# Kernel optimization log

Hardware: AMD Instinct MI355X
Metric: run time of the kernel (lower is better)

The kernel has to match this reference:

```python
import jax, jax.numpy as jnp
import numpy as np

DIM = 256
NUM_HEADS = 4
WINDOW = 64
EPS = 1e-6


def setup_inputs() -> dict:
    key = jax.random.key(0)
    ks = jax.random.split(key, 12)
    d = DIM
    s = 0.02
    return {
        "x": jax.random.normal(ks[0], (4, 2049, d), dtype=jnp.float32),
        "norm1_w": jnp.ones((d,), jnp.float32),
        "in_proj_w": jax.random.normal(ks[1], (3 * d, d), jnp.float32) * s,
        "in_proj_b": jnp.zeros((3 * d,), jnp.float32),
        "out_proj_w": jax.random.normal(ks[2], (d, d), jnp.float32) * s,
        "out_proj_b": jnp.zeros((d,), jnp.float32),
        "norm2_w": jnp.ones((d,), jnp.float32),
        "w1": jax.random.normal(ks[3], (2 * d, d), jnp.float32) * s,
        "b1": jnp.zeros((2 * d,), jnp.float32),
        "w2": jax.random.normal(ks[4], (d, 2 * d), jnp.float32) * s,
        "b2": jnp.zeros((d,), jnp.float32),
    }


def _rmsnorm(x, w):
    r = jax.lax.rsqrt(jnp.mean(x * x, axis=-1, keepdims=True) + EPS)
    return x * r * w


def _factorized_mask(size):
    # global token 0 attends/attended everywhere; others banded within WINDOW
    idx = jnp.arange(size)
    band = jnp.abs(idx[:, None] - idx[None, :]) <= WINDOW
    allowed = band | (idx[:, None] == 0) | (idx[None, :] == 0)
    return jnp.where(allowed, 0.0, -jnp.inf).astype(jnp.float32)


def reference(x, norm1_w, in_proj_w, in_proj_b, out_proj_w, out_proj_b,
              norm2_w, w1, b1, w2, b2):
    B, S, D = x.shape
    H = NUM_HEADS
    dh = D // H
    residual = x
    h = _rmsnorm(x, norm1_w)
    # fused qkv projection (torch MHA in_proj): [B,S,3D]
    qkv = h @ in_proj_w.T + in_proj_b
    q, k, v = jnp.split(qkv, 3, axis=-1)
    q = q.reshape(B, S, H, dh).transpose(0, 2, 1, 3)  # [B,H,S,dh]
    k = k.reshape(B, S, H, dh).transpose(0, 2, 1, 3)
    v = v.reshape(B, S, H, dh).transpose(0, 2, 1, 3)
    scores = jnp.einsum("bhqd,bhkd->bhqk", q, k) / jnp.sqrt(jnp.float32(dh))
    scores = scores + _factorized_mask(S)  # additive -inf mask
    attn = jax.nn.softmax(scores, axis=-1)
    ctx = jnp.einsum("bhqk,bhkd->bhqd", attn, v)
    ctx = ctx.transpose(0, 2, 1, 3).reshape(B, S, D)
    attn_out = ctx @ out_proj_w.T + out_proj_b
    x1 = residual + attn_out
    h2 = _rmsnorm(x1, norm2_w)
    ffn = jax.nn.gelu(h2 @ w1.T + b1, approximate=False) @ w2.T + b2
    return x1 + ffn
```

## Files before the change

kernel.cpp:

```cpp
#include <hip/hip_runtime.h>
#include <hip/hip_bf16.h>
#include <math.h>

#define BATCH 4
#define SEQ 2049
#define DIMD 256
#define NHEAD 4
#define DH 64
#define WIN 64
#define M_ROWS (BATCH * SEQ)
#define M_PAD 8320

#define QBLK 33
#define NKB 10
#define PSTR 168
#define VGUARD 64
#define VW 2256

#define NSPLIT 33
#define TBLK 576

typedef __attribute__((ext_vector_type(8))) short short8;
typedef __attribute__((ext_vector_type(4))) float f32x4;
typedef __hip_bfloat16 bf16;

__device__ __forceinline__ float b2f(short u) {
    union { unsigned int i; float f; } c;
    c.i = ((unsigned int)(unsigned short)u) << 16;
    return c.f;
}
__device__ __forceinline__ short f2b(float f) {
    bf16 h = __float2bfloat16(f);
    return *reinterpret_cast<short*>(&h);
}

__global__ __launch_bounds__(256) void prep_kernel(
        const float* __restrict__ wq, const float* __restrict__ wo,
        const float* __restrict__ w1, const float* __restrict__ w2,
        bf16* __restrict__ oq, bf16* __restrict__ oo,
        bf16* __restrict__ o1, bf16* __restrict__ o2,
        const float* __restrict__ x, const float* __restrict__ nw,
        bf16* __restrict__ h) {
    const int bi = blockIdx.x, tid = threadIdx.x;
    if (bi < 2048) {
        int i = bi * 256 + tid;
        if (i < 196608)      oq[i]          = __float2bfloat16(wq[i]);
        else if (i < 262144) oo[i - 196608] = __float2bfloat16(wo[i - 196608]);
        else if (i < 393216) o1[i - 262144] = __float2bfloat16(w1[i - 262144]);
        else                 o2[i - 393216] = __float2bfloat16(w2[i - 393216]);
        return;
    }
    int wid = tid >> 6, lane = tid & 63;
    int row = (bi - 2048) * 4 + wid;
    if (row >= M_ROWS) return;
    const float4 v = reinterpret_cast<const float4*>(x + (size_t)row * DIMD)[lane];
    float ss = v.x * v.x + v.y * v.y + v.z * v.z + v.w * v.w;
    #pragma unroll
    for (int o = 1; o < 64; o <<= 1) ss += __shfl_xor(ss, o, 64);
    float r = rsqrtf(ss * (1.0f / DIMD) + 1e-6f);
    const float4 wv = reinterpret_cast<const float4*>(nw)[lane];
    bf16* hp = h + (size_t)row * DIMD + lane * 4;
    hp[0] = __float2bfloat16(v.x * r * wv.x);
    hp[1] = __float2bfloat16(v.y * r * wv.y);
    hp[2] = __float2bfloat16(v.z * r * wv.z);
    hp[3] = __float2bfloat16(v.w * r * wv.w);
}

__global__ __launch_bounds__(256) void rmsnorm_kernel(const float* __restrict__ x,
        const float* __restrict__ w, bf16* __restrict__ h, int M) {
    int wid = threadIdx.x >> 6, lane = threadIdx.x & 63;
    int row = blockIdx.x * 4 + wid;
    if (row >= M) return;
    const float4 v = reinterpret_cast<const float4*>(x + (size_t)row * DIMD)[lane];
    float ss = v.x * v.x + v.y * v.y + v.z * v.z + v.w * v.w;
    #pragma unroll
    for (int o = 1; o < 64; o <<= 1) ss += __shfl_xor(ss, o, 64);
    float r = rsqrtf(ss * (1.0f / DIMD) + 1e-6f);
    const float4 wv = reinterpret_cast<const float4*>(w)[lane];
    bf16* hp = h + (size_t)row * DIMD + lane * 4;
    hp[0] = __float2bfloat16(v.x * r * wv.x);
    hp[1] = __float2bfloat16(v.y * r * wv.y);
    hp[2] = __float2bfloat16(v.z * r * wv.z);
    hp[3] = __float2bfloat16(v.w * r * wv.w);
}

template<int MODE, int BN>
__global__ __launch_bounds__(256) void gemm_lds(
        const bf16* __restrict__ A, const bf16* __restrict__ B,
        const float* __restrict__ bias, const float* __restrict__ resid,
        void* __restrict__ C, int M, int N, int K) {
    constexpr int FN = BN / 32;
    __shared__ __align__(16) short lA[8 * 128 * 8];
    __shared__ __align__(16) short lB[8 * BN * 8];
    const int tid = threadIdx.x, lane = tid & 63, wid = tid >> 6;
    const int m0 = blockIdx.x * 128;
    const int n0 = blockIdx.y * BN;
    const int wr = wid >> 1, wc = wid & 1;
    const int r = lane & 15, g = lane >> 4;

    f32x4 acc[4][FN];
    #pragma unroll
    for (int i = 0; i < 4; i++)
        #pragma unroll
        for (int j = 0; j < FN; j++) acc[i][j] = (f32x4){0.f, 0.f, 0.f, 0.f};

    for (int k0 = 0; k0 < K; k0 += 64) {
        #pragma unroll
        for (int it = 0; it < 4; ++it) {
            int c = it * 256 + tid;
            int kc = c >> 7, row = c & 127;
            __builtin_amdgcn_global_load_lds(
                (const __attribute__((address_space(1))) void*)(A + (size_t)(m0 + row) * K + k0 + kc * 8),
                (__attribute__((address_space(3))) void*)&lA[c * 8], 16, 0, 0);
        }
        #pragma unroll
        for (int it = 0; it < BN / 32; ++it) {
            int c = it * 256 + tid;
            int kc = c / BN, row = c % BN;
            __builtin_amdgcn_global_load_lds(
                (const __attribute__((address_space(1))) void*)(B + (size_t)(n0 + row) * K + k0 + kc * 8),
                (__attribute__((address_space(3))) void*)&lB[c * 8], 16, 0, 0);
        }
        __syncthreads();

        #pragma unroll
        for (int kk = 0; kk < 2; kk++) {
            short8 a[4], b[FN];
            #pragma unroll
            for (int mi = 0; mi < 4; mi++)
                a[mi] = *reinterpret_cast<const short8*>(&lA[((kk * 4 + g) * 128 + wr * 64 + mi * 16 + r) * 8]);
            #pragma unroll
            for (int ni = 0; ni < FN; ni++)
                b[ni] = *reinterpret_cast<const short8*>(&lB[((kk * 4 + g) * BN + wc * (BN / 2) + ni * 16 + r) * 8]);
            #pragma unroll
            for (int mi = 0; mi < 4; mi++)
                #pragma unroll
                for (int ni = 0; ni < FN; ni++)
                    acc[mi][ni] = __builtin_amdgcn_mfma_f32_16x16x32_bf16(a[mi], b[ni], acc[mi][ni], 0, 0, 0);
        }
        __syncthreads();
    }

    const int c0 = lane & 15, r0 = (lane >> 4) * 4;
    #pragma unroll
    for (int mi = 0; mi < 4; mi++) {
        #pragma unroll
        for (int ni = 0; ni < FN; ni++) {
            int col = n0 + wc * (BN / 2) + ni * 16 + c0;
            float bv = bias[col];
            #pragma unroll
            for (int j = 0; j < 4; j++) {
                int row = m0 + wr * 64 + mi * 16 + r0 + j;
                if (row < M) {
                    float v = acc[mi][ni][j] + bv;
                    if (MODE == 2) v = 0.5f * v * (1.0f + erff(v * 0.70710678118654752f));
                    if (MODE == 1) {
                        v += resid[(size_t)row * N + col];
                        reinterpret_cast<float*>(C)[(size_t)row * N + col] = v;
                    } else {
                        reinterpret_cast<bf16*>(C)[(size_t)row * N + col] = __float2bfloat16(v);
                    }
                }
            }
        }
    }
}

__global__ __launch_bounds__(256) void trans_partial(const short* __restrict__ qkv,
                                                     short* __restrict__ vT,
                                                     float* __restrict__ part) {
    const int tid = threadIdx.x;
    if (blockIdx.x < TBLK) {
        __shared__ short tl[64][72];
        const int jt = blockIdx.x % 36, bh = blockIdx.x / 36;
        const int b = bh >> 2, h = bh & 3;
        const size_t rbase = (size_t)b * SEQ;
        const int cbase = jt * 64;
        #pragma unroll
        for (int it = 0; it < 2; it++) {
            int idx = it * 256 + tid;
            int jj = idx >> 3, dg = (idx & 7) * 8;
            int j = cbase + jj - VGUARD;
            short8 v = (short8){0, 0, 0, 0, 0, 0, 0, 0};
            if (j >= 0 && j < SEQ)
                v = *reinterpret_cast<const short8*>(qkv + (rbase + j) * 768 + 512 + h * 64 + dg);
            *reinterpret_cast<short8*>(&tl[jj][dg]) = v;
        }
        __syncthreads();
        #pragma unroll
        for (int it = 0; it < 2; it++) {
            int idx = it * 256 + tid;
            int d = idx >> 3, jg = (idx & 7) * 8;
            int c = cbase + jg;
            if (c + 8 <= VW) {
                short8 o;
                #pragma unroll
                for (int e = 0; e < 8; e++) o[e] = tl[jg + e][d];
                *reinterpret_cast<short8*>(vT + ((size_t)bh * 64 + d) * VW + c) = o;
            }
        }
        return;
    }
    __shared__ float q_s[64];
    __shared__ float p_s[64];
    __shared__ float meta[2];
    __shared__ float osum[4][64];
    const int idx = blockIdx.x - TBLK;
    const int bh = idx / NSPLIT, s = idx % NSPLIT;
    const int b = bh >> 2, h = bh & 3;
    const size_t base = (size_t)b * SEQ;
    const int j0 = s * 64;
    const int lane = tid & 63, wid = tid >> 6;

    if (tid < 64) q_s[tid] = b2f(qkv[base * 768 + h * 64 + tid]);
    __syncthreads();

    if (wid == 0) {
        int j = j0 + lane;
        float sc = -1e30f;
        if (j < SEQ) {
            const short8* kp = reinterpret_cast<const short8*>(qkv + (base + j) * 768 + 256 + h * 64);
            float acc = 0.f;
            #pragma unroll
            for (int d8 = 0; d8 < 8; ++d8) {
                short8 kv = kp[d8];
                #pragma unroll
                for (int e = 0; e < 8; ++e) acc += q_s[d8 * 8 + e] * b2f(kv[e]);
            }
            sc = acc * 0.125f;
        }
        float mx = sc;
        #pragma unroll
        for (int o = 1; o < 64; o <<= 1) mx = fmaxf(mx, __shfl_xor(mx, o, 64));
        float p = (j < SEQ) ? expf(sc - mx) : 0.f;
        p_s[lane] = p;
        float l = p;
        #pragma unroll
        for (int o = 1; o < 64; o <<= 1) l += __shfl_xor(l, o, 64);
        if (lane == 0) { meta[0] = mx; meta[1] = l; }
    }
    __syncthreads();

    float oa = 0.f;
    #pragma unroll
    for (int i0 = 0; i0 < 16; i0++) {
        int i = wid + i0 * 4;
        if (j0 + i < SEQ) oa += p_s[i] * b2f(qkv[(base + j0 + i) * 768 + 512 + h * 64 + lane]);
    }
    osum[wid][lane] = oa;
    __syncthreads();
    if (wid == 0) {
        float o = osum[0][lane] + osum[1][lane] + osum[2][lane] + osum[3][lane];
        float* pp = part + (size_t)(bh * NSPLIT + s) * 66;
        pp[lane] = o;
        if (lane == 0) { pp[64] = meta[0]; pp[65] = meta[1]; }
    }
}

__global__ __launch_bounds__(256) void attn_band_mfma(const short* __restrict__ qkv,
                                                      const short* __restrict__ vT,
                                                      const float* __restrict__ part,
                                                      short* __restrict__ ctx) {
    __shared__ short p_lds[4][16][PSTR];
    const int tid = threadIdx.x, lane = tid & 63, wid = tid >> 6;
    const int qb = blockIdx.x % QBLK;
    const int bh = blockIdx.x / QBLK;
    const int b = bh >> 2, h = bh & 3;
    const size_t rbase = (size_t)b * SEQ;
    const int q0w = qb * 64 + wid * 16;
    const int jbase = q0w - 64;
    const int lrow = lane & 15;
    const int koff = (lane >> 4) * 8;
    const int c0 = lrow, r0 = (lane >> 4) * 4;

    int qrow = q0w + lrow; if (qrow > SEQ - 1) qrow = SEQ - 1;
    const short* qp = qkv + (rbase + qrow) * 768 + h * 64;
    short8 aq0 = *reinterpret_cast<const short8*>(qp + koff);
    short8 aq1 = *reinterpret_cast<const short8*>(qp + 32 + koff);

    const short* k0p = qkv + rbase * 768 + 256 + h * 64;
    short8 k0a = *reinterpret_cast<const short8*>(k0p + koff);
    short8 k0b = *reinterpret_cast<const short8*>(k0p + 32 + koff);
    float s0 = 0.f;
    #pragma unroll
    for (int e = 0; e < 8; e++)
        s0 += b2f(aq0[e]) * b2f(k0a[e]) + b2f(aq1[e]) * b2f(k0b[e]);
    s0 += __shfl_xor(s0, 16, 64);
    s0 += __shfl_xor(s0, 32, 64);

    f32x4 s[NKB];
    #pragma unroll
    for (int n = 0; n < NKB; n++) {
        int j = jbase + n * 16 + lrow;
        int jc = j < 0 ? 0 : (j > SEQ - 1 ? SEQ - 1 : j);
        const short* kp = qkv + (rbase + jc) * 768 + 256 + h * 64;
        short8 bk0 = *reinterpret_cast<const short8*>(kp + koff);
        short8 bk1 = *reinterpret_cast<const short8*>(kp + 32 + koff);
        f32x4 acc = (f32x4){0.f, 0.f, 0.f, 0.f};
        acc = __builtin_amdgcn_mfma_f32_16x16x32_bf16(aq0, bk0, acc, 0, 0, 0);
        acc = __builtin_amdgcn_mfma_f32_16x16x32_bf16(aq1, bk1, acc, 0, 0, 0);
        s[n] = acc;
    }

    const float SC = 0.125f * 1.44269504088896340736f;
    const bool g1 = (jbase > 0);
    float s0q[4], m4[4];
    #pragma unroll
    for (int jj = 0; jj < 4; jj++) {
        s0q[jj] = __shfl(s0, r0 + jj, 64) * SC;
        m4[jj] = g1 ? s0q[jj] : -1e30f;
    }
    #pragma unroll
    for (int n = 0; n < NKB; n++) {
        int j = jbase + n * 16 + c0;
        bool jv = (j >= 0) && (j < SEQ);
        #pragma unroll
        for (int jj = 0; jj < 4; jj++) {
            int q = q0w + r0 + jj;
            int dd = q - j; if (dd < 0) dd = -dd;
            bool allowed = jv && (dd <= WIN || j == 0);
            float v = allowed ? s[n][jj] * SC : -1e30f;
            s[n][jj] = v;
            m4[jj] = fmaxf(m4[jj], v);
        }
    }
    #pragma unroll
    for (int o = 1; o < 16; o <<= 1) {
        #pragma unroll
        for (int jj = 0; jj < 4; jj++) m4[jj] = fmaxf(m4[jj], __shfl_xor(m4[jj], o, 64));
    }

    float p0[4], l4[4];
    #pragma unroll
    for (int jj = 0; jj < 4; jj++) {
        p0[jj] = g1 ? exp2f(s0q[jj] - m4[jj]) : 0.f;
        l4[jj] = p0[jj];
    }
    #pragma unroll
    for (int n = 0; n < NKB; n++) {
        #pragma unroll
        for (int jj = 0; jj < 4; jj++) {
            float p = exp2f(s[n][jj] - m4[jj]);
            l4[jj] += p;
            p_lds[wid][r0 + jj][n * 16 + c0] = f2b(p);
        }
    }
    #pragma unroll
    for (int o = 1; o < 16; o <<= 1) {
        #pragma unroll
        for (int jj = 0; jj < 4; jj++) l4[jj] += __shfl_xor(l4[jj], o, 64);
    }

    __syncthreads();

    f32x4 o[4];
    #pragma unroll
    for (int dn = 0; dn < 4; dn++) o[dn] = (f32x4){0.f, 0.f, 0.f, 0.f};
    #pragma unroll
    for (int ks = 0; ks < NKB / 2; ks++) {
        short8 ap = *reinterpret_cast<const short8*>(&p_lds[wid][lrow][ks * 32 + koff]);
        int cc = VGUARD + jbase + ks * 32 + koff;
        #pragma unroll
        for (int dn = 0; dn < 4; dn++) {
            short8 bv = *reinterpret_cast<const short8*>(
                vT + ((size_t)bh * 64 + dn * 16 + lrow) * VW + cc);
            o[dn] = __builtin_amdgcn_mfma_f32_16x16x32_bf16(ap, bv, o[dn], 0, 0, 0);
        }
    }

    #pragma unroll
    for (int jj = 0; jj < 4; jj++) {
        int q = q0w + r0 + jj;
        if (q >= 1 && q < SEQ) {
            float rl = 1.0f / l4[jj];
            #pragma unroll
            for (int dn = 0; dn < 4; dn++) {
                float v0 = b2f(qkv[rbase * 768 + 512 + h * 64 + dn * 16 + c0]);
                float val = (o[dn][jj] + p0[jj] * v0) * rl;
                ctx[(rbase + q) * 256 + h * 64 + dn * 16 + c0] = f2b(val);
            }
        }
    }

    if (qb == 0) {
        __syncthreads();
        if (wid == 0) {
            float m = (lane < NSPLIT) ? part[(size_t)(bh * NSPLIT + lane) * 66 + 64] : -1e30f;
            #pragma unroll
            for (int o2 = 1; o2 < 64; o2 <<= 1) m = fmaxf(m, __shfl_xor(m, o2, 64));
            float L = 0.f, ov = 0.f;
            for (int sp = 0; sp < NSPLIT; sp++) {
                const float* pp = part + (size_t)(bh * NSPLIT + sp) * 66;
                float w = expf(pp[64] - m);
                L += pp[65] * w;
                ov += pp[lane] * w;
            }
            ctx[rbase * 256 + h * 64 + lane] = f2b(ov / L);
        }
    }
}

extern "C" void kernel_launch(void* const* d_in, const int* in_sizes, int n_in,
                              void* d_out, int out_size, void* d_ws, size_t ws_size,
                              hipStream_t stream) {
    const float* x         = (const float*)d_in[0];
    const float* norm1_w   = (const float*)d_in[1];
    const float* in_proj_w = (const float*)d_in[2];
    const float* in_proj_b = (const float*)d_in[3];
    const float* out_proj_w= (const float*)d_in[4];
    const float* out_proj_b= (const float*)d_in[5];
    const float* norm2_w   = (const float*)d_in[6];
    const float* w1        = (const float*)d_in[7];
    const float* b1        = (const float*)d_in[8];
    const float* w2        = (const float*)d_in[9];
    const float* b2        = (const float*)d_in[10];
    float* out = (float*)d_out;

    const int M = M_ROWS;
    char* ws = (char*)d_ws;
    size_t off = 0;
    auto take = [&](size_t bytes) {
        char* p = ws + off;
        off = (off + bytes + 255) & ~(size_t)255;
        return p;
    };
    bf16* h_bf   = (bf16*)take((size_t)M_PAD * 256 * 2);
    bf16* qkv_bf = (bf16*)take((size_t)M_PAD * 768 * 2);
    bf16* ctx_bf = (bf16*)take((size_t)M_PAD * 256 * 2);
    float* x1    = (float*)take((size_t)M_PAD * 256 * 4);
    bf16* h2_bf  = (bf16*)take((size_t)M_PAD * 256 * 2);
    bf16* g_bf   = (bf16*)take((size_t)M_PAD * 512 * 2);
    bf16* wq_bf  = (bf16*)take(768 * 256 * 2);
    bf16* wo_bf  = (bf16*)take(256 * 256 * 2);
    bf16* w1_bf  = (bf16*)take(512 * 256 * 2);
    bf16* w2_bf  = (bf16*)take(256 * 512 * 2);
    float* part  = (float*)take((size_t)16 * NSPLIT * 66 * 4);
    short* vT    = (short*)take((size_t)16 * 64 * VW * 2);
    (void)ws_size; (void)in_sizes; (void)n_in; (void)out_size;

    prep_kernel<<<dim3(2048 + 2049), dim3(256), 0, stream>>>(
        in_proj_w, out_proj_w, w1, w2, wq_bf, wo_bf, w1_bf, w2_bf, x, norm1_w, h_bf);
    gemm_lds<0, 128><<<dim3(65, 6), dim3(256), 0, stream>>>(h_bf, wq_bf, in_proj_b, (const float*)nullptr,
                                                            (void*)qkv_bf, M, 768, 256);
    trans_partial<<<dim3(TBLK + 16 * NSPLIT), dim3(256), 0, stream>>>(
        (const short*)qkv_bf, vT, part);
    attn_band_mfma<<<dim3(16 * QBLK), dim3(256), 0, stream>>>(
        (const short*)qkv_bf, vT, part, (short*)ctx_bf);
    gemm_lds<1, 64><<<dim3(65, 4), dim3(256), 0, stream>>>(ctx_bf, wo_bf, out_proj_b, x,
                                                           (void*)x1, M, 256, 256);
    rmsnorm_kernel<<<dim3((M + 3) / 4), dim3(256), 0, stream>>>(x1, norm2_w, h2_bf, M);
    gemm_lds<2, 128><<<dim3(65, 4), dim3(256), 0, stream>>>(h2_bf, w1_bf, b1, (const float*)nullptr,
                                                            (void*)g_bf, M, 512, 256);
    gemm_lds<1, 64><<<dim3(65, 4), dim3(256), 0, stream>>>(g_bf, w2_bf, b2, x1,
                                                           (void*)out, M, 256, 512);
}
```

Measured before the change: 124.9 us.

## Fuse V transpose into QKV GEMM epilogue and RMSNorm into out-proj GEMM

The QKV GEMM epilogue now writes V straight into the transposed, guard-padded vT layout and writes Q/K to a narrower 512-wide buffer. This removes the separate transpose pass, and prep_kernel zeroes vT beforehand so the guard regions stay valid. The out-projection GEMM now uses full-row 32x256 tiles, so it can compute the residual add and the second RMSNorm in its epilogue, which drops the standalone rmsnorm kernel. In exchange, the V stores are scattered and uncoalesced, the out-proj grid has fewer blocks with a larger B tile per block, and prep does extra zeroing work.

New measurement: 127.8 us. +2.3%, slower.

```diff
diff --git a/kernel.cpp b/kernel.cpp
--- a/kernel.cpp
+++ b/kernel.cpp
@@ -5,8 +5,6 @@
 #define BATCH 4
 #define SEQ 2049
 #define DIMD 256
-#define NHEAD 4
-#define DH 64
 #define WIN 64
 #define M_ROWS (BATCH * SEQ)
 #define M_PAD 8320
@@ -16,9 +14,10 @@
 #define PSTR 168
 #define VGUARD 64
 #define VW 2256
+#define QKSTR 512
 
 #define NSPLIT 33
-#define TBLK 576
+#define VT_F4 288768
 
 typedef __attribute__((ext_vector_type(8))) short short8;
 typedef __attribute__((ext_vector_type(4))) float f32x4;
@@ -40,7 +39,7 @@
         bf16* __restrict__ oq, bf16* __restrict__ oo,
         bf16* __restrict__ o1, bf16* __restrict__ o2,
         const float* __restrict__ x, const float* __restrict__ nw,
-        bf16* __restrict__ h) {
+        bf16* __restrict__ h, float4* __restrict__ vTz) {
     const int bi = blockIdx.x, tid = threadIdx.x;
     if (bi < 2048) {
         int i = bi * 256 + tid;
@@ -50,6 +49,15 @@
         else                 o2[i - 393216] = __float2bfloat16(w2[i - 393216]);
         return;
     }
+    if (bi >= 4097) {
+        int zi = (bi - 4097) * 256 + tid;
+        #pragma unroll
+        for (int it = 0; it < 3; it++) {
+            int idx = zi + it * 512 * 256;
+            if (idx < VT_F4) vTz[idx] = (float4){0.f, 0.f, 0.f, 0.f};
+        }
+        return;
+    }
     int wid = tid >> 6, lane = tid & 63;
     int row = (bi - 2048) * 4 + wid;
     if (row >= M_ROWS) return;
@@ -66,22 +74,86 @@
     hp[3] = __float2bfloat16(v.w * r * wv.w);
 }
 
-__global__ __launch_bounds__(256) void rmsnorm_kernel(const float* __restrict__ x,
-        const float* __restrict__ w, bf16* __restrict__ h, int M) {
-    int wid = threadIdx.x >> 6, lane = threadIdx.x & 63;
-    int row = blockIdx.x * 4 + wid;
-    if (row >= M) return;
-    const float4 v = reinterpret_cast<const float4*>(x + (size_t)row * DIMD)[lane];
-    float ss = v.x * v.x + v.y * v.y + v.z * v.z + v.w * v.w;
-    #pragma unroll
-    for (int o = 1; o < 64; o <<= 1) ss += __shfl_xor(ss, o, 64);
-    float r = rsqrtf(ss * (1.0f / DIMD) + 1e-6f);
-    const float4 wv = reinterpret_cast<const float4*>(w)[lane];
-    bf16* hp = h + (size_t)row * DIMD + lane * 4;
-    hp[0] = __float2bfloat16(v.x * r * wv.x);
-    hp[1] = __float2bfloat16(v.y * r * wv.y);
-    hp[2] = __float2bfloat16(v.z * r * wv.z);
-    hp[3] = __float2bfloat16(v.w * r * wv.w);
+__global__ __launch_bounds__(256) void gemm_qkv(
+        const bf16* __restrict__ A, const bf16* __restrict__ B,
+        const float* __restrict__ bias, bf16* __restrict__ qk, short* __restrict__ vT) {
+    __shared__ __align__(16) short lA[8 * 128 * 8];
+    __shared__ __align__(16) short lB[8 * 128 * 8];
+    const int tid = threadIdx.x, lane = tid & 63, wid = tid >> 6;
+    const int m0 = blockIdx.x * 128;
+    const int n0 = blockIdx.y * 128;
+    const int wr = wid >> 1, wc = wid & 1;
+    const int r = lane & 15, g = lane >> 4;
+    const int K = 256;
+
+    f32x4 acc[4][4];
+    #pragma unroll
+    for (int i = 0; i < 4; i++)
+        #pragma unroll
+        for (int j = 0; j < 4; j++) acc[i][j] = (f32x4){0.f, 0.f, 0.f, 0.f};
+
+    for (int k0 = 0; k0 < K; k0 += 64) {
+        #pragma unroll
+        for (int it = 0; it < 4; ++it) {
+            int c = it * 256 + tid;
+            int kc = c >> 7, row = c & 127;
+            __builtin_amdgcn_global_load_lds(
+                (const __attribute__((address_space(1))) void*)(A + (size_t)(m0 + row) * K + k0 + kc * 8),
+                (__attribute__((address_space(3))) void*)&lA[c * 8], 16, 0, 0);
+        }
+        #pragma unroll
+        for (int it = 0; it < 4; ++it) {
+            int c = it * 256 + tid;
+            int kc = c >> 7, row = c & 127;
+            __builtin_amdgcn_global_load_lds(
+                (const __attribute__((address_space(1))) void*)(B + (size_t)(n0 + row) * K + k0 + kc * 8),
+                (__attribute__((address_space(3))) void*)&lB[c * 8], 16, 0, 0);
+        }
+        __syncthreads();
+        #pragma unroll
+        for (int kk = 0; kk < 2; kk++) {
+            short8 a[4], b[4];
+            #pragma unroll
+            for (int mi = 0; mi < 4; mi++)
+                a[mi] = *reinterpret_cast<const short8*>(&lA[((kk * 4 + g) * 128 + wr * 64 + mi * 16 + r) * 8]);
+            #pragma unroll
+            for (int ni = 0; ni < 4; ni++)
+                b[ni] = *reinterpret_cast<const short8*>(&lB[((kk * 4 + g) * 128 + wc * 64 + ni * 16 + r) * 8]);
+            #pragma unroll
+            for (int mi = 0; mi < 4; mi++)
+                #pragma unroll
+                for (int ni = 0; ni < 4; ni++)
+                    acc[mi][ni] = __builtin_amdgcn_mfma_f32_16x16x32_bf16(a[mi], b[ni], acc[mi][ni], 0, 0, 0);
+        }
+        __syncthreads();
+    }
+
+    const int c0 = lane & 15, r0 = (lane >> 4) * 4;
+    const bool isV = (n0 >= 512);
+    #pragma unroll
+    for (int mi = 0; mi < 4; mi++) {
+        #pragma unroll
+        for (int ni = 0; ni < 4; ni++) {
+            int col = n0 + wc * 64 + ni * 16 + c0;
+            float bv = bias[col];
+            #pragma unroll
+            for (int j = 0; j < 4; j++) {
+                int row = m0 + wr * 64 + mi * 16 + r0 + j;
+                if (row < M_ROWS) {
+                    float v = acc[mi][ni][j] + bv;
+                    if (!isV) {
+                        qk[(size_t)row * QKSTR + col] = __float2bfloat16(v);
+                    } else {
+                        int dcol = col - 512, hh = dcol >> 6, d = dcol & 63;
+                        int bb = row >> 11;
+                        int js = row - bb * SEQ;
+                        if (js < 0) { bb--; js += SEQ; }
+                        vT[((size_t)((bb * 4 + hh) * 64 + d)) * VW + VGUARD + js] = f2b(v);
+                    }
+                }
+            }
+        }
+    }
 }
 
 template<int MODE, int BN>
@@ -122,7 +194,6 @@
                 (__attribute__((address_space(3))) void*)&lB[c * 8], 16, 0, 0);
         }
         __syncthreads();
-
         #pragma unroll
         for (int kk = 0; kk < 2; kk++) {
             short8 a[4], b[FN];
@@ -166,60 +237,138 @@
     }
 }
 
-__global__ __launch_bounds__(256) void trans_partial(const short* __restrict__ qkv,
-                                                     short* __restrict__ vT,
-                                                     float* __restrict__ part) {
-    const int tid = threadIdx.x;
-    if (blockIdx.x < TBLK) {
-        __shared__ short tl[64][72];
-        const int jt = blockIdx.x % 36, bh = blockIdx.x / 36;
-        const int b = bh >> 2, h = bh & 3;
-        const size_t rbase = (size_t)b * SEQ;
-        const int cbase = jt * 64;
-        #pragma unroll
-        for (int it = 0; it < 2; it++) {
-            int idx = it * 256 + tid;
-            int jj = idx >> 3, dg = (idx & 7) * 8;
-            int j = cbase + jj - VGUARD;
-            short8 v = (short8){0, 0, 0, 0, 0, 0, 0, 0};
-            if (j >= 0 && j < SEQ)
-                v = *reinterpret_cast<const short8*>(qkv + (rbase + j) * 768 + 512 + h * 64 + dg);
-            *reinterpret_cast<short8*>(&tl[jj][dg]) = v;
+__global__ __launch_bounds__(256) void gemm_or(
+        const bf16* __restrict__ A, const bf16* __restrict__ B,
+        const float* __restrict__ bias, const float* __restrict__ resid,
+        const float* __restrict__ nw,
+        float* __restrict__ x1, bf16* __restrict__ h2) {
+    __shared__ __align__(16) short lA[8 * 32 * 8];
+    __shared__ __align__(16) short lB[8 * 256 * 8];
+    __shared__ float osq[4][32];
+    const int tid = threadIdx.x, lane = tid & 63, wid = tid >> 6;
+    const int m0 = blockIdx.x * 32;
+    const int wc = wid;
+    const int r = lane & 15, g = lane >> 4;
+    const int K = 256;
+
+    f32x4 acc[2][4];
+    #pragma unroll
+    for (int i = 0; i < 2; i++)
+        #pragma unroll
+        for (int j = 0; j < 4; j++) acc[i][j] = (f32x4){0.f, 0.f, 0.f, 0.f};
+
+    for (int k0 = 0; k0 < K; k0 += 64) {
+        {
+            int c = tid;
+            int kc = c >> 5, row = c & 31;
+            __builtin_amdgcn_global_load_lds(
+                (const __attribute__((address_space(1))) void*)(A + (size_t)(m0 + row) * K + k0 + kc * 8),
+                (__attribute__((address_space(3))) void*)&lA[c * 8], 16, 0, 0);
+        }
+        #pragma unroll
+        for (int it = 0; it < 8; ++it) {
+            int c = it * 256 + tid;
+            int kc = c >> 8, row = c & 255;
+            __builtin_amdgcn_global_load_lds(
+                (const __attribute__((address_space(1))) void*)(B + (size_t)row * K + k0 + kc * 8),
+                (__attribute__((address_space(3))) void*)&lB[c * 8], 16, 0, 0);
         }
         __syncthreads();
         #pragma unroll
-        for (int it = 0; it < 2; it++) {
-            int idx = it * 256 + tid;
-            int d = idx >> 3, jg = (idx & 7) * 8;
-            int c = cbase + jg;
-            if (c + 8 <= VW) {
-                short8 o;
+        for (int kk = 0; kk < 2; kk++) {
+            short8 a[2], b[4];
+            #pragma unroll
+            for (int mi = 0; mi < 2; mi++)
+                a[mi] = *reinterpret_cast<const short8*>(&lA[((kk * 4 + g) * 32 + mi * 16 + r) * 8]);
+            #pragma unroll
+            for (int ni = 0; ni < 4; ni++)
+                b[ni] = *reinterpret_cast<const short8*>(&lB[((kk * 4 + g) * 256 + wc * 64 + ni * 16 + r) * 8]);
+            #pragma unroll
+            for (int mi = 0; mi < 2; mi++)
                 #pragma unroll
-                for (int e = 0; e < 8; e++) o[e] = tl[jg + e][d];
-                *reinterpret_cast<short8*>(vT + ((size_t)bh * 64 + d) * VW + c) = o;
+                for (int ni = 0; ni < 4; ni++)
+                    acc[mi][ni] = __builtin_amdgcn_mfma_f32_16x16x32_bf16(a[mi], b[ni], acc[mi][ni], 0, 0, 0);
+        }
+        __syncthreads();
+    }
+
+    const int c0 = lane & 15, r0 = (lane >> 4) * 4;
+    float ssq[2][4];
+    #pragma unroll
+    for (int mi = 0; mi < 2; mi++) {
+        #pragma unroll
+        for (int j = 0; j < 4; j++) {
+            int row = m0 + mi * 16 + r0 + j;
+            float s = 0.f;
+            if (row < M_ROWS) {
+                #pragma unroll
+                for (int ni = 0; ni < 4; ni++) {
+                    int col = wc * 64 + ni * 16 + c0;
+                    float v = acc[mi][ni][j] + bias[col] + resid[(size_t)row * 256 + col];
+                    acc[mi][ni][j] = v;
+                    x1[(size_t)row * 256 + col] = v;
+                    s += v * v;
+                }
             }
-        }
-        return;
-    }
+            ssq[mi][j] = s;
+        }
+    }
+    #pragma unroll
+    for (int o = 1; o < 16; o <<= 1) {
+        #pragma unroll
+        for (int mi = 0; mi < 2; mi++)
+            #pragma unroll
+            for (int j = 0; j < 4; j++) ssq[mi][j] += __shfl_xor(ssq[mi][j], o, 64);
+    }
+    if (c0 == 0) {
+        #pragma unroll
+        for (int mi = 0; mi < 2; mi++)
+            #pragma unroll
+            for (int j = 0; j < 4; j++) osq[wc][mi * 16 + r0 + j] = ssq[mi][j];
+    }
+    __syncthreads();
+    #pragma unroll
+    for (int mi = 0; mi < 2; mi++) {
+        #pragma unroll
+        for (int j = 0; j < 4; j++) {
+            int lr = mi * 16 + r0 + j;
+            int row = m0 + lr;
+            if (row < M_ROWS) {
+                float tot = osq[0][lr] + osq[1][lr] + osq[2][lr] + osq[3][lr];
+                float rs = rsqrtf(tot * (1.0f / 256.0f) + 1e-6f);
+                #pragma unroll
+                for (int ni = 0; ni < 4; ni++) {
+                    int col = wc * 64 + ni * 16 + c0;
+                    h2[(size_t)row * 256 + col] = __float2bfloat16(acc[mi][ni][j] * rs * nw[col]);
+                }
+            }
+        }
+    }
+}
+
+__global__ __launch_bounds__(256) void attn_partial(const bf16* __restrict__ qk,
+                                                    const short* __restrict__ vT,
+                                                    float* __restrict__ part) {
     __shared__ float q_s[64];
     __shared__ float p_s[64];
     __shared__ float meta[2];
     __shared__ float osum[4][64];
-    const int idx = blockIdx.x - TBLK;
-    const int bh = idx / NSPLIT, s = idx % NSPLIT;
+    const int tid = threadIdx.x;
+    const int bh = blockIdx.x / NSPLIT, s = blockIdx.x % NSPLIT;
     const int b = bh >> 2, h = bh & 3;
     const size_t base = (size_t)b * SEQ;
     const int j0 = s * 64;
     const int lane = tid & 63, wid = tid >> 6;
 
-    if (tid < 64) q_s[tid] = b2f(qkv[base * 768 + h * 64 + tid]);
+    if (tid < 64) q_s[tid] = __bfloat162float(qk[base * QKSTR + h * 64 + tid]);
     __syncthreads();
 
     if (wid == 0) {
         int j = j0 + lane;
         float sc = -1e30f;
         if (j < SEQ) {
-            const short8* kp = reinterpret_cast<const short8*>(qkv + (base + j) * 768 + 256 + h * 64);
+            const short8* kp = reinterpret_cast<const short8*>(
+                reinterpret_cast<const short*>(qk) + (base + j) * QKSTR + 256 + h * 64);
             float acc = 0.f;
             #pragma unroll
             for (int d8 = 0; d8 < 8; ++d8) {
@@ -241,11 +390,12 @@
     }
     __syncthreads();
 
+    const short* vrow = vT + ((size_t)bh * 64 + lane) * VW + VGUARD + j0;
     float oa = 0.f;
     #pragma unroll
     for (int i0 = 0; i0 < 16; i0++) {
         int i = wid + i0 * 4;
-        if (j0 + i < SEQ) oa += p_s[i] * b2f(qkv[(base + j0 + i) * 768 + 512 + h * 64 + lane]);
+        if (j0 + i < SEQ) oa += p_s[i] * b2f(vrow[i]);
     }
     osum[wid][lane] = oa;
     __syncthreads();
@@ -257,11 +407,12 @@
     }
 }
 
-__global__ __launch_bounds__(256) void attn_band_mfma(const short* __restrict__ qkv,
+__global__ __launch_bounds__(256) void attn_band_mfma(const bf16* __restrict__ qkb,
                                                       const short* __restrict__ vT,
                                                       const float* __restrict__ part,
                                                       short* __restrict__ ctx) {
     __shared__ short p_lds[4][16][PSTR];
+    const short* qk = reinterpret_cast<const short*>(qkb);
     const int tid = threadIdx.x, lane = tid & 63, wid = tid >> 6;
     const int qb = blockIdx.x % QBLK;
     const int bh = blockIdx.x / QBLK;
@@ -274,11 +425,11 @@
     const int c0 = lrow, r0 = (lane >> 4) * 4;
 
     int qrow = q0w + lrow; if (qrow > SEQ - 1) qrow = SEQ - 1;
-    const short* qp = qkv + (rbase + qrow) * 768 + h * 64;
+    const short* qp = qk + (rbase + qrow) * QKSTR + h * 64;
     short8 aq0 = *reinterpret_cast<const short8*>(qp + koff);
     short8 aq1 = *reinterpret_cast<const short8*>(qp + 32 + koff);
 
-    const short* k0p = qkv + rbase * 768 + 256 + h * 64;
+    const short* k0p = qk + rbase * QKSTR + 256 + h * 64;
     short8 k0a = *reinterpret_cast<const short8*>(k0p + koff);
     short8 k0b = *reinterpret_cast<const short8*>(k0p + 32 + koff);
     float s0 = 0.f;
@@ -293,7 +444,7 @@
     for (int n = 0; n < NKB; n++) {
         int j = jbase + n * 16 + lrow;
         int jc = j < 0 ? 0 : (j > SEQ - 1 ? SEQ - 1 : j);
-        const short* kp = qkv + (rbase + jc) * 768 + 256 + h * 64;
+        const short* kp = qk + (rbase + jc) * QKSTR + 256 + h * 64;
         short8 bk0 = *reinterpret_cast<const short8*>(kp + koff);
         short8 bk1 = *reinterpret_cast<const short8*>(kp + 32 + koff);
         f32x4 acc = (f32x4){0.f, 0.f, 0.f, 0.f};
@@ -375,7 +526,7 @@
             float rl = 1.0f / l4[jj];
             #pragma unroll
             for (int dn = 0; dn < 4; dn++) {
-                float v0 = b2f(qkv[rbase * 768 + 512 + h * 64 + dn * 16 + c0]);
+                float v0 = b2f(vT[((size_t)bh * 64 + dn * 16 + c0) * VW + VGUARD]);
                 float val = (o[dn][jj] + p0[jj] * v0) * rl;
                 ctx[(rbase + q) * 256 + h * 64 + dn * 16 + c0] = f2b(val);
             }
@@ -425,7 +576,7 @@
         return p;
     };
     bf16* h_bf   = (bf16*)take((size_t)M_PAD * 256 * 2);
-    bf16* qkv_bf = (bf16*)take((size_t)M_PAD * 768 * 2);
+    bf16* qk_bf  = (bf16*)take((size_t)M_PAD * QKSTR * 2);
     bf16* ctx_bf = (bf16*)take((size_t)M_PAD * 256 * 2);
     float* x1    = (float*)take((size_t)M_PAD * 256 * 4);
     bf16* h2_bf  = (bf16*)take((size_t)M_PAD * 256 * 2);
@@ -438,17 +589,13 @@
     short* vT    = (short*)take((size_t)16 * 64 * VW * 2);
     (void)ws_size; (void)in_sizes; (void)n_in; (void)out_size;
 
-    prep_kernel<<<dim3(2048 + 2049), dim3(256), 0, stream>>>(
-        in_proj_w, out_proj_w, w1, w2, wq_bf, wo_bf, w1_bf, w2_bf, x, norm1_w, h_bf);
-    gemm_lds<0, 128><<<dim3(65, 6), dim3(256), 0, stream>>>(h_bf, wq_bf, in_proj_b, (const float*)nullptr,
-                                                            (void*)qkv_bf, M, 768, 256);
-    trans_partial<<<dim3(TBLK + 16 * NSPLIT), dim3(256), 0, stream>>>(
-        (const short*)qkv_bf, vT, part);
-    attn_band_mfma<<<dim3(16 * QBLK), dim3(256), 0, stream>>>(
-        (const short*)qkv_bf, vT, part, (short*)ctx_bf);
-    gemm_lds<1, 64><<<dim3(65, 4), dim3(256), 0, stream>>>(ctx_bf, wo_bf, out_proj_b, x,
-                                                           (void*)x1, M, 256, 256);
-    rmsnorm_kernel<<<dim3((M + 3) / 4), dim3(256), 0, stream>>>(x1, norm2_w, h2_bf, M);
+    prep_kernel<<<dim3(4609), dim3(256), 0, stream>>>(
+        in_proj_w, out_proj_w, w1, w2, wq_bf, wo_bf, w1_bf, w2_bf,
+        x, norm1_w, h_bf, (float4*)vT);
+    gemm_qkv<<<dim3(65, 6), dim3(256), 0, stream>>>(h_bf, wq_bf, in_proj_b, qk_bf, vT);
+    attn_partial<<<dim3(16 * NSPLIT), dim3(256), 0, stream>>>(qk_bf, vT, part);
+    attn_band_mfma<<<dim3(16 * QBLK), dim3(256), 0, stream>>>(qk_bf, vT, part, (short*)ctx_bf);
+    gemm_or<<<dim3(257), dim3(256), 0, stream>>>(ctx_bf, wo_bf, out_proj_b, x, norm2_w, x1, h2_bf);
     gemm_lds<2, 128><<<dim3(65, 4), dim3(256), 0, stream>>>(h2_bf, w1_bf, b1, (const float*)nullptr,
                                                             (void*)g_bf, M, 512, 256);
     gemm_lds<1, 64><<<dim3(65, 4), dim3(256), 0, stream>>>(g_bf, w2_bf, b2, x1,
```
